# Kernel tuning notes

Hardware: AMD Instinct MI355X
Metric: run time of the kernel (lower is better)

Reference implementation:

```python
import jax, jax.numpy as jnp
import numpy as np

B, S, HID = 1, 4096, 2048
H, KVH, D = 8, 4, 256
QR, KR, VR = 6, 2, 2
WINDOW = 1024
SOFTCAP = 50.0
SCALING = 256.0 ** -0.5  # query_pre_attn_scalar ** -0.5
EPS = 1e-6
NEG = -2.3819763e38


def _rope(x, cos, sin):
    # x: [B,S,R,D]; cos/sin: [S,D//2] -> rotate interleaved complex pairs
    xr = x.reshape(*x.shape[:-1], D // 2, 2)
    x1, x2 = xr[..., 0], xr[..., 1]
    c = cos[None, :, None, :]
    s = sin[None, :, None, :]
    out = jnp.stack([x1 * c - x2 * s, x1 * s + x2 * c], axis=-1)
    return out.reshape(x.shape)


def _rmsnorm(x, w):
    var = jnp.mean(x * x, axis=-1, keepdims=True)
    return x * jax.lax.rsqrt(var + EPS) * (1.0 + w)


def setup_inputs() -> dict:
    key = jax.random.key(0)
    ks = jax.random.split(key, 12)
    sc = HID ** -0.5
    pos = np.arange(S, dtype=np.float32)
    inv = 1.0 / (10000.0 ** (np.arange(0, D, 2, dtype=np.float32) / D))
    fr = pos[:, None] * inv[None, :]
    return {
        'hidden_states': jax.random.normal(ks[0], (B, S, HID), jnp.float32),
        'freqs_cos': jnp.asarray(np.cos(fr), jnp.float32),
        'freqs_sin': jnp.asarray(np.sin(fr), jnp.float32),
        'W_A_q': jax.random.normal(ks[1], (H * QR, HID), jnp.float32) * sc,
        'W_A_k': jax.random.normal(ks[2], (KVH * KR, HID), jnp.float32) * sc,
        'W_A_v': jax.random.normal(ks[3], (KVH * VR, HID), jnp.float32) * sc,
        'W_B_q': jax.random.normal(ks[4], (QR * D, HID), jnp.float32) * sc,
        'W_B_k': jax.random.normal(ks[5], (KR * D, HID), jnp.float32) * sc,
        'W_B_v': jax.random.normal(ks[6], (VR * D, HID), jnp.float32) * sc,
        'W_o': jax.random.normal(ks[7], (HID, H * D), jnp.float32) * (H * D) ** -0.5,
        'q_norm_w': jnp.zeros((D,), jnp.float32),
        'k_norm_w': jnp.zeros((D,), jnp.float32),
        'k_cache_A': jnp.zeros((B, S, KVH, KR), jnp.float32),
        'k_cache_B': jnp.zeros((B, S, KR, D), jnp.float32),
        'v_cache_A': jnp.zeros((B, S, KVH, VR), jnp.float32),
        'v_cache_B': jnp.zeros((B, S, VR, D), jnp.float32),
        'kv_write_indices': jnp.arange(S, dtype=jnp.int32),
    }


def reference(hidden_states, freqs_cos, freqs_sin, W_A_q, W_A_k, W_A_v,
              W_B_q, W_B_k, W_B_v, W_o, q_norm_w, k_norm_w,
              k_cache_A, k_cache_B, v_cache_A, v_cache_B, kv_write_indices):
    x = hidden_states  # [B,S,HID]
    # factorized projections
    A_q = (x @ W_A_q.T).reshape(B, S, H, QR)
    A_k = (x @ W_A_k.T).reshape(B, S, KVH, KR)
    A_v = (x @ W_A_v.T).reshape(B, S, KVH, VR)
    B_q = (x @ W_B_q.T).reshape(B, S, QR, D)
    B_k = (x @ W_B_k.T).reshape(B, S, KR, D)
    B_v = (x @ W_B_v.T).reshape(B, S, VR, D)
    # RoPE on head-dim factors of Q and K
    B_q = _rope(B_q, freqs_cos, freqs_sin)
    B_k = _rope(B_k, freqs_cos, freqs_sin)
    # write factors into the TPA KV cache
    k_cache_A = k_cache_A.at[:, kv_write_indices].set(A_k)
    k_cache_B = k_cache_B.at[:, kv_write_indices].set(B_k)
    v_cache_A = v_cache_A.at[:, kv_write_indices].set(A_v)
    v_cache_B = v_cache_B.at[:, kv_write_indices].set(B_v)
    # reconstruct Q/K/V from rank-R tensor products (mean over rank)
    q = jnp.einsum('bshr,bsrd->bshd', A_q, B_q) / QR          # [B,S,H,D]
    k = jnp.einsum('btkr,btrd->btkd', k_cache_A, k_cache_B) / KR  # [B,T,KVH,D]
    v = jnp.einsum('btkr,btrd->btkd', v_cache_A, v_cache_B) / VR
    # QK RMSNorm
    q = _rmsnorm(q, q_norm_w)
    k = _rmsnorm(k, k_norm_w)
    # GQA: expand KV heads to query heads
    rep = H // KVH
    k = jnp.repeat(k, rep, axis=2)  # [B,T,H,D]
    v = jnp.repeat(v, rep, axis=2)
    # scores with softcapping + sliding-window causal mask
    scores = jnp.einsum('bshd,bthd->bhst', q * SCALING, k)
    scores = jnp.tanh(scores / SOFTCAP) * SOFTCAP
    q_pos = kv_write_indices[:, None]        # [S,1]
    k_pos = jnp.arange(S, dtype=jnp.int32)[None, :]  # [1,T]
    diff = q_pos - k_pos
    allowed = (diff >= 0) & (diff < WINDOW)
    scores = jnp.where(allowed[None, None], scores, NEG)
    probs = jax.nn.softmax(scores, axis=-1)
    out = jnp.einsum('bhst,bthd->bshd', probs, v).reshape(B, S, H * D)
    return out @ W_o.T
```

## Files before the change

kernel.cpp:

```cpp
#include <hip/hip_runtime.h>
#include <hip/hip_bf16.h>
#include <cstdint>
#include <cstddef>

constexpr int SEQ   = 4096;
constexpr int HIDN  = 2048;
constexpr int NHEAD = 8;
constexpr int NKVH  = 4;
constexpr int DH    = 256;
constexpr int NPROJ = 2624;
constexpr int NPROJP= 2816;
constexpr int WIN   = 1024;

typedef __attribute__((ext_vector_type(4))) float f32x4;
typedef __attribute__((ext_vector_type(8))) short bf16x8;
typedef unsigned short u16;

__device__ __forceinline__ u16 f2bf(float x) {
  union { float f; uint32_t u; } v; v.f = x;
  uint32_t r = v.u + 0x7fffu + ((v.u >> 16) & 1u);
  return (u16)(r >> 16);
}
__device__ __forceinline__ float bf2f(u16 v) {
  union { uint32_t u; float f; } w; w.u = (uint32_t)v << 16; return w.f;
}

__device__ __forceinline__ uint32_t cvtpk(float lo, float hi) {
  uint32_t r;
  asm("v_cvt_pk_bf16_f32 %0, %1, %2" : "=v"(r) : "v"(lo), "v"(hi));
  return r;
}

__device__ __forceinline__ void gl_lds16(const u16* g, u16* l) {
  __builtin_amdgcn_global_load_lds(
      (const __attribute__((address_space(1))) uint32_t*)g,
      (__attribute__((address_space(3))) uint32_t*)l, 16, 0, 0);
}

__device__ __forceinline__ void sync_vm() {
  asm volatile("s_waitcnt vmcnt(0)" ::: "memory");
  __builtin_amdgcn_s_barrier();
  __builtin_amdgcn_sched_barrier(0);
}

__device__ __forceinline__ void phase_barrier() {
  asm volatile("" ::: "memory");
  __builtin_amdgcn_s_barrier();
  __builtin_amdgcn_sched_barrier(0);
}

__device__ __forceinline__ int xcd_swz(int wg, int nwg) {
  const int q = nwg >> 3, r = nwg & 7;
  const int xcd = wg & 7, lo = wg >> 3;
  return (xcd < r ? xcd * (q + 1) : r * (q + 1) + (xcd - r) * q) + lo;
}

__global__ __launch_bounds__(256) void k_cvt(const float* __restrict__ src,
                                             u16* __restrict__ dst, int n4) {
  int i = blockIdx.x * 256 + threadIdx.x;
  if (i >= n4) return;
  float4 v = ((const float4*)src)[i];
  ushort4 o; o.x = f2bf(v.x); o.y = f2bf(v.y); o.z = f2bf(v.z); o.w = f2bf(v.w);
  ((ushort4*)dst)[i] = o;
}

__global__ __launch_bounds__(256) void k_wcat(
    const float* __restrict__ waq, const float* __restrict__ wak,
    const float* __restrict__ wav, const float* __restrict__ wbq,
    const float* __restrict__ wbk, const float* __restrict__ wbv,
    u16* __restrict__ wcat) {
  const int r = blockIdx.x;
  const int col0 = threadIdx.x * 8;
  u16* out = wcat + (size_t)r * HIDN + col0;
  const float* src = nullptr; int rr = 0;
  if      (r < 48)   { src = waq; rr = r; }
  else if (r < 56)   { src = wak; rr = r - 48; }
  else if (r < 64)   { src = wav; rr = r - 56; }
  else if (r < 1600) { src = wbq; rr = r - 64; }
  else if (r < 2112) { src = wbk; rr = r - 1600; }
  else if (r < 2624) { src = wbv; rr = r - 2112; }
  if (!src) {
    ushort4 z = {0,0,0,0}; ((ushort4*)out)[0] = z; ((ushort4*)out)[1] = z; return;
  }
  const float* s = src + (size_t)rr * HIDN + col0;
#pragma unroll
  for (int i = 0; i < 2; ++i) {
    float4 v = ((const float4*)s)[i];
    ushort4 o; o.x = f2bf(v.x); o.y = f2bf(v.y); o.z = f2bf(v.z); o.w = f2bf(v.w);
    ((ushort4*)out)[i] = o;
  }
}

template<int OBF16>
__global__ __launch_bounds__(512, 2)
void k_gemm256(const u16* __restrict__ A, const u16* __restrict__ Bm,
               void* __restrict__ Cv, int M, int N, int K) {
  __shared__ u16 lA[2][256 * 64];
  __shared__ u16 lB[2][256 * 64];
  const int tid = threadIdx.x;
  const int wid = tid >> 6, lane = tid & 63;
  const int l15 = lane & 15, g = lane >> 4;
  const int wr = wid >> 2, wc = wid & 3;
  const int nwg = gridDim.x * gridDim.y;
  int wg = xcd_swz(blockIdx.y * gridDim.x + blockIdx.x, nwg);
  const int m0 = (wg / gridDim.x) * 256, n0 = (wg % gridDim.x) * 256;

  f32x4 acc[8][4];
#pragma unroll
  for (int m = 0; m < 8; ++m)
#pragma unroll
    for (int n = 0; n < 4; ++n) acc[m][n] = (f32x4){0.f,0.f,0.f,0.f};
  const int NT = K >> 6;

  const int srow = tid >> 3;
  const int scc  = (tid & 7) ^ (srow & 7);
  const u16* ag = A  + (size_t)(m0 + srow) * K + scc * 8;
  const u16* bg = Bm + (size_t)(n0 + srow) * K + scc * 8;

  auto stB = [&](int buf, int kt) {
    const size_t ko = (size_t)kt << 6;
#pragma unroll
    for (int j = 0; j < 4; ++j)
      gl_lds16(bg + (size_t)(j*64) * K + ko, &lB[buf][j*4096 + wid*512]);
  };
  auto stA0 = [&](int buf, int kt) {
    const size_t ko = (size_t)kt << 6;
    gl_lds16(ag + ko,                   &lA[buf][wid*512]);
    gl_lds16(ag + (size_t)64 * K + ko,  &lA[buf][4096 + wid*512]);
  };
  auto stA1 = [&](int buf, int kt) {
    const size_t ko = (size_t)kt << 6;
    gl_lds16(ag + (size_t)128 * K + ko, &lA[buf][8192  + wid*512]);
    gl_lds16(ag + (size_t)192 * K + ko, &lA[buf][12288 + wid*512]);
  };

  const int sw8 = l15 & 7;
  int aoff[2], boff[2];
#pragma unroll
  for (int kk = 0; kk < 2; ++kk) {
    aoff[kk] = (wr*128 + l15)*64 + (((kk*4 + g) ^ sw8) << 3);
    boff[kk] = (wc*64  + l15)*64 + (((kk*4 + g) ^ sw8) << 3);
  }
  const u16* lAf = &lA[0][0];
  const u16* lBf = &lB[0][0];

  stB(0, 0); stA0(0, 0); stA1(0, 0);

  for (int t = 0; t < NT; ++t) {
    const int buf = t & 1, nb = buf ^ 1;
    const int ab = buf * 16384, bb = buf * 16384;
    const bool more = (t + 1 < NT);
    bf16x8 af[8], f0, f1;

    if (more) {
      stB(nb, t + 1);
      asm volatile("s_waitcnt vmcnt(4)" ::: "memory");
    } else {
      asm volatile("s_waitcnt vmcnt(0)" ::: "memory");
    }
    __builtin_amdgcn_s_barrier();
    __builtin_amdgcn_sched_barrier(0);
#pragma unroll
    for (int m = 0; m < 8; ++m) af[m] = *(const bf16x8*)&lAf[ab + aoff[0] + m*1024];
    f0 = *(const bf16x8*)&lBf[bb + boff[0]];
    f1 = *(const bf16x8*)&lBf[bb + boff[0] + 1024];
    __builtin_amdgcn_s_setprio(1);
#pragma unroll
    for (int m = 0; m < 8; ++m) {
      acc[m][0] = __builtin_amdgcn_mfma_f32_16x16x32_bf16(af[m], f0, acc[m][0], 0, 0, 0);
      acc[m][1] = __builtin_amdgcn_mfma_f32_16x16x32_bf16(af[m], f1, acc[m][1], 0, 0, 0);
    }
    __builtin_amdgcn_s_setprio(0);
    phase_barrier();

    f0 = *(const bf16x8*)&lBf[bb + boff[0] + 2048];
    f1 = *(const bf16x8*)&lBf[bb + boff[0] + 3072];
    if (more) stA0(nb, t + 1);
    phase_barrier();
    __builtin_amdgcn_s_setprio(1);
#pragma unroll
    for (int m = 0; m < 8; ++m) {
      acc[m][2] = __builtin_amdgcn_mfma_f32_16x16x32_bf16(af[m], f0, acc[m][2], 0, 0, 0);
      acc[m][3] = __builtin_amdgcn_mfma_f32_16x16x32_bf16(af[m], f1, acc[m][3], 0, 0, 0);
    }
    __builtin_amdgcn_s_setprio(0);
    phase_barrier();

#pragma unroll
    for (int m = 0; m < 8; ++m) af[m] = *(const bf16x8*)&lAf[ab + aoff[1] + m*1024];
    f0 = *(const bf16x8*)&lBf[bb + boff[1]];
    f1 = *(const bf16x8*)&lBf[bb + boff[1] + 1024];
    if (more) stA1(nb, t + 1);
    phase_barrier();
    __builtin_amdgcn_s_setprio(1);
#pragma unroll
    for (int m = 0; m < 8; ++m) {
      acc[m][0] = __builtin_amdgcn_mfma_f32_16x16x32_bf16(af[m], f0, acc[m][0], 0, 0, 0);
      acc[m][1] = __builtin_amdgcn_mfma_f32_16x16x32_bf16(af[m], f1, acc[m][1], 0, 0, 0);
    }
    __builtin_amdgcn_s_setprio(0);
    phase_barrier();

    f0 = *(const bf16x8*)&lBf[bb + boff[1] + 2048];
    f1 = *(const bf16x8*)&lBf[bb + boff[1] + 3072];
    phase_barrier();
    __builtin_amdgcn_s_setprio(1);
#pragma unroll
    for (int m = 0; m < 8; ++m) {
      acc[m][2] = __builtin_amdgcn_mfma_f32_16x16x32_bf16(af[m], f0, acc[m][2], 0, 0, 0);
      acc[m][3] = __builtin_amdgcn_mfma_f32_16x16x32_bf16(af[m], f1, acc[m][3], 0, 0, 0);
    }
    __builtin_amdgcn_s_setprio(0);
    phase_barrier();
  }

#pragma unroll
  for (int m = 0; m < 8; ++m)
#pragma unroll
    for (int n = 0; n < 4; ++n)
#pragma unroll
      for (int j = 0; j < 4; ++j) {
        const int row = m0 + wr*128 + m*16 + g*4 + j;
        const int col = n0 + wc*64 + n*16 + l15;
        if constexpr (OBF16) ((u16*)Cv)[(size_t)row * N + col] = f2bf(acc[m][n][j]);
        else                 ((float*)Cv)[(size_t)row * N + col] = acc[m][n][j];
      }
}

__global__ __launch_bounds__(256)
void k_qkv(const u16* __restrict__ Y, const float* __restrict__ cosT,
           const float* __restrict__ sinT, const float* __restrict__ qw,
           const float* __restrict__ kw, u16* __restrict__ q_s,
           u16* __restrict__ k_s, u16* __restrict__ v_s) {
  const int s = blockIdx.x;
  const int d = threadIdx.x;
  __shared__ float row[NPROJ];
  __shared__ float red[12][4];
  const u16* yr = Y + (size_t)s * NPROJP;
  for (int u4 = d; u4 < NPROJ/4; u4 += 256) {
    ushort4 v4 = ((const ushort4*)yr)[u4];
    row[u4*4+0] = bf2f(v4.x); row[u4*4+1] = bf2f(v4.y);
    row[u4*4+2] = bf2f(v4.z); row[u4*4+3] = bf2f(v4.w);
  }
  __syncthreads();
  const int i = d >> 1;
  const float cf = cosT[s * 128 + i];
  const float sf = sinT[s * 128 + i];
  const bool odd = d & 1;
  float bq[6], bk[2], bv[2];
#pragma unroll
  for (int r = 0; r < 6; ++r) {
    float x1 = row[64 + r*256 + 2*i], x2 = row[64 + r*256 + 2*i + 1];
    bq[r] = odd ? (x1*sf + x2*cf) : (x1*cf - x2*sf);
  }
#pragma unroll
  for (int r = 0; r < 2; ++r) {
    float x1 = row[1600 + r*256 + 2*i], x2 = row[1600 + r*256 + 2*i + 1];
    bk[r] = odd ? (x1*sf + x2*cf) : (x1*cf - x2*sf);
    bv[r] = row[2112 + r*256 + d];
  }
  float qv[8], kv[4], vv[4];
#pragma unroll
  for (int h = 0; h < 8; ++h) {
    float a = 0.f;
#pragma unroll
    for (int r = 0; r < 6; ++r) a += row[h*6 + r] * bq[r];
    qv[h] = a * (1.0f / 6.0f);
  }
#pragma unroll
  for (int c = 0; c < 4; ++c) {
    kv[c] = (row[48 + c*2]*bk[0] + row[48 + c*2 + 1]*bk[1]) * 0.5f;
    vv[c] = (row[56 + c*2]*bv[0] + row[56 + c*2 + 1]*bv[1]) * 0.5f;
  }
  const int lane = d & 63, wv = d >> 6;
#pragma unroll
  for (int t = 0; t < 12; ++t) {
    float x = (t < 8) ? qv[t] : kv[t - 8];
    float ss = x * x;
#pragma unroll
    for (int off = 32; off > 0; off >>= 1) ss += __shfl_xor(ss, off);
    if (lane == 0) red[t][wv] = ss;
  }
  __syncthreads();
  const float qwf = 1.0f + qw[d], kwf = 1.0f + kw[d];
#pragma unroll
  for (int h = 0; h < 8; ++h) {
    float v = red[h][0] + red[h][1] + red[h][2] + red[h][3];
    float r = rsqrtf(v * (1.0f/256.0f) + 1e-6f);
    q_s[((size_t)s*8 + h)*256 + d] = f2bf(qv[h] * r * qwf * 0.0625f);
  }
#pragma unroll
  for (int c = 0; c < 4; ++c) {
    float v = red[8+c][0] + red[8+c][1] + red[8+c][2] + red[8+c][3];
    float r = rsqrtf(v * (1.0f/256.0f) + 1e-6f);
    k_s[((size_t)s*4 + c)*256 + d] = f2bf(kv[c] * r * kwf);
    v_s[((size_t)s*4 + c)*256 + d] = f2bf(vv[c]);
  }
}

__global__ __launch_bounds__(256)
void k_vt(const u16* __restrict__ v_s, u16* __restrict__ vT) {
  __shared__ u16 tile[64][72];
  const int s0 = blockIdx.x * 64, d0 = blockIdx.y * 64, c = blockIdx.z;
  const int tid = threadIdx.x;
#pragma unroll
  for (int it = 0; it < 2; ++it) {
    const int u = it * 256 + tid;
    const int r = u >> 3, cc = u & 7;
    const u16* s = &v_s[(((size_t)(s0 + r))*4 + c)*256 + d0 + cc*8];
    ushort4 a = *(const ushort4*)s, b = *(const ushort4*)(s + 4);
    tile[r][cc*8+0]=a.x; tile[r][cc*8+1]=a.y; tile[r][cc*8+2]=a.z; tile[r][cc*8+3]=a.w;
    tile[r][cc*8+4]=b.x; tile[r][cc*8+5]=b.y; tile[r][cc*8+6]=b.z; tile[r][cc*8+7]=b.w;
  }
  __syncthreads();
#pragma unroll
  for (int it = 0; it < 2; ++it) {
    const int u = it * 256 + tid;
    const int dr = u >> 3, sc = u & 7;
    ushort4 a, b;
    a.x = tile[sc*8+0][dr]; a.y = tile[sc*8+1][dr]; a.z = tile[sc*8+2][dr]; a.w = tile[sc*8+3][dr];
    b.x = tile[sc*8+4][dr]; b.y = tile[sc*8+5][dr]; b.z = tile[sc*8+6][dr]; b.w = tile[sc*8+7][dr];
    u16* o = vT + ((size_t)c*256 + d0 + dr)*SEQ + s0 + sc*8;
    *(ushort4*)o = a; *(ushort4*)(o + 4) = b;
  }
}

__global__ __launch_bounds__(512, 2)
void k_attn(const u16* __restrict__ q_s, const u16* __restrict__ k_s,
            const u16* __restrict__ vT, const int* __restrict__ idx,
            u16* __restrict__ ao) {
  __shared__ u16 Kt[2][64 * 256];
  __shared__ u16 Vt[2][256 * 64];
  __shared__ u16 Pb[8][16 * 68];
  const int b = blockIdx.x;
  const int c = b & 3, qt = b >> 2;
  const int q0 = qt * 64;
  const int tid = threadIdx.x;
  const int wid = tid >> 6, lane = tid & 63;
  const int l15 = lane & 15, g = lane >> 4;
  const int h = 2*c + (wid >> 2);
  const int qsub = wid & 3;
  const int qrow = q0 + qsub*16 + l15;
  const int qpos = idx[qrow];

  bf16x8 qf[8];
  const u16* qb = q_s + ((size_t)qrow * 8 + h) * 256;
#pragma unroll
  for (int kk = 0; kk < 8; ++kk) qf[kk] = *(const bf16x8*)(qb + kk*32 + g*8);

  const int sw = l15 & 7;
  int kbase[8];
#pragma unroll
  for (int kk = 0; kk < 8; ++kk)
    kbase[kk] = l15*256 + ((((kk<<2)+g) ^ sw) << 3);
  u16* KtF = &Kt[0][0];
  u16* VtF = &Vt[0][0];
  u16* Pw  = &Pb[wid][0];

  f32x4 accO[16];
#pragma unroll
  for (int n = 0; n < 16; ++n) accO[n] = (f32x4){0.f,0.f,0.f,0.f};
  float mrun = -50.0f, lrun = 0.0f;

  int t0 = q0 - (WIN - 1); if (t0 < 0) t0 = 0;
  const int kt_lo = t0 >> 6, kt_hi = qt;

  const u16* kgp = k_s + (size_t)(kt_lo*64 + (tid>>5)) * 1024 + c*256
                   + (((tid & 31) ^ ((tid >> 5) & 7)) << 3);
  const u16* vgp = vT + (size_t)c*1048576 + (size_t)(tid>>3)*4096 + kt_lo*64
                   + (((tid & 7) ^ ((tid >> 3) & 7)) << 3);

  auto stage = [&](int buf) {
#pragma unroll
    for (int i = 0; i < 4; ++i)
      gl_lds16(kgp + i*16384,  &Kt[buf][(i*512 + wid*64) * 8]);
#pragma unroll
    for (int i = 0; i < 4; ++i)
      gl_lds16(vgp + i*262144, &Vt[buf][(i*512 + wid*64) * 8]);
  };

  stage(0);
  int cur = 0;
  for (int kt = kt_lo; kt <= kt_hi; ++kt) {
    const int k0 = kt << 6;
    sync_vm();
    if (kt < kt_hi) { kgp += 65536; vgp += 64; stage(cur ^ 1); }

    const int kco = cur * 16384;
    f32x4 sc[4];
#pragma unroll
    for (int nk = 0; nk < 4; ++nk) sc[nk] = (f32x4){0.f,0.f,0.f,0.f};
    __builtin_amdgcn_s_setprio(1);
#pragma unroll
    for (int nk = 0; nk < 4; ++nk)
#pragma unroll
      for (int kk = 0; kk < 8; ++kk) {
        bf16x8 kf = *(const bf16x8*)&KtF[kco + nk*4096 + kbase[kk]];
        sc[nk] = __builtin_amdgcn_mfma_f32_16x16x32_bf16(kf, qf[kk], sc[nk], 0, 0, 0);
      }
    __builtin_amdgcn_s_setprio(0);

    float tv[16];
#pragma unroll
    for (int nk = 0; nk < 4; ++nk)
#pragma unroll
      for (int j = 0; j < 4; ++j) {
        float u = __builtin_amdgcn_exp2f(sc[nk][j] * 0.05770780163555854f);
        tv[nk*4+j] = fmaf(-100.0f, __builtin_amdgcn_rcpf(1.0f + u), 50.0f);
      }
    if (kt == kt_hi) {
#pragma unroll
      for (int nk = 0; nk < 4; ++nk)
#pragma unroll
        for (int j = 0; j < 4; ++j)
          if (k0 + nk*16 + g*4 + j > qpos) tv[nk*4+j] = -1e38f;
    } else if (kt == kt_lo) {
#pragma unroll
      for (int nk = 0; nk < 4; ++nk)
#pragma unroll
        for (int j = 0; j < 4; ++j)
          if (qpos - (k0 + nk*16 + g*4 + j) > 1023) tv[nk*4+j] = -1e38f;
    }

    float tmax = tv[0];
#pragma unroll
    for (int t = 1; t < 16; ++t) tmax = fmaxf(tmax, tv[t]);
    if (__any(tmax > mrun + 8.0f)) {
      float tq = fmaxf(tmax, __shfl_xor(tmax, 16));
      tq = fmaxf(tq, __shfl_xor(tq, 32));
      const float mnew = fmaxf(mrun, tq);
      const float scale = __builtin_amdgcn_exp2f((mrun - mnew) * 1.442695041f);
      float scj[4];
#pragma unroll
      for (int j = 0; j < 4; ++j) scj[j] = __shfl(scale, g*4 + j);
#pragma unroll
      for (int n = 0; n < 16; ++n) {
        accO[n][0] *= scj[0]; accO[n][1] *= scj[1];
        accO[n][2] *= scj[2]; accO[n][3] *= scj[3];
      }
      lrun *= scale;
      mrun = mnew;
    }
    const float mr2 = mrun * 1.442695041f;
    float p[16];
#pragma unroll
    for (int t = 0; t < 16; ++t) {
      p[t] = __builtin_amdgcn_exp2f(fmaf(tv[t], 1.442695041f, -mr2));
      lrun += p[t];
    }

#pragma unroll
    for (int nk = 0; nk < 4; ++nk) {
      uint2 w = { cvtpk(p[nk*4+0], p[nk*4+1]), cvtpk(p[nk*4+2], p[nk*4+3]) };
      *(uint2*)&Pw[l15*68 + nk*16 + g*4] = w;
    }
    const int vco = cur * 16384;
    __builtin_amdgcn_s_setprio(1);
#pragma unroll
    for (int half = 0; half < 2; ++half) {
      bf16x8 pa = *(const bf16x8*)&Pw[l15*68 + half*32 + g*8];
#pragma unroll
      for (int n = 0; n < 16; ++n) {
        bf16x8 vf = *(const bf16x8*)&VtF[vco + (n*16 + l15)*64
                                         + ((((half<<2)+g) ^ sw) << 3)];
        accO[n] = __builtin_amdgcn_mfma_f32_16x16x32_bf16(pa, vf, accO[n], 0, 0, 0);
      }
    }
    __builtin_amdgcn_s_setprio(0);
    cur ^= 1;
  }

  lrun += __shfl_xor(lrun, 16);
  lrun += __shfl_xor(lrun, 32);
  const float linv = __builtin_amdgcn_rcpf(lrun);
  float lj[4];
#pragma unroll
  for (int j = 0; j < 4; ++j) lj[j] = __shfl(linv, g*4 + j);
#pragma unroll
  for (int n = 0; n < 16; ++n)
#pragma unroll
    for (int j = 0; j < 4; ++j) {
      const int r = q0 + qsub*16 + g*4 + j;
      ao[(size_t)r * HIDN + h*256 + n*16 + l15] = f2bf(accO[n][j] * lj[j]);
    }
}

extern "C" void kernel_launch(void* const* d_in, const int* in_sizes, int n_in,
                              void* d_out, int out_size, void* d_ws, size_t ws_size,
                              hipStream_t stream) {
  const float* x    = (const float*)d_in[0];
  const float* fcos = (const float*)d_in[1];
  const float* fsin = (const float*)d_in[2];
  const float* waq  = (const float*)d_in[3];
  const float* wak  = (const float*)d_in[4];
  const float* wav  = (const float*)d_in[5];
  const float* wbq  = (const float*)d_in[6];
  const float* wbk  = (const float*)d_in[7];
  const float* wbv  = (const float*)d_in[8];
  const float* wo   = (const float*)d_in[9];
  const float* qnw  = (const float*)d_in[10];
  const float* knw  = (const float*)d_in[11];
  const int*   idx  = (const int*)d_in[16];
  float* out = (float*)d_out;

  char* p = (char*)d_ws;
  u16*  xb   = (u16*)p;                 p += (size_t)SEQ*HIDN*2;
  u16*  wcat = (u16*)p;                 p += (size_t)NPROJP*HIDN*2;
  u16*  wob  = (u16*)p;                 p += (size_t)HIDN*HIDN*2;
  u16*  ypr  = (u16*)p;                 p += (size_t)SEQ*NPROJP*2;
  u16*  q_s  = (u16*)p;                 p += (size_t)SEQ*NHEAD*DH*2;
  u16*  k_s  = (u16*)p;                 p += (size_t)SEQ*NKVH*DH*2;
  u16*  v_s  = (u16*)p;                 p += (size_t)SEQ*NKVH*DH*2;
  u16*  vT   = (u16*)p;                 p += (size_t)SEQ*NKVH*DH*2;
  u16*  ao   = (u16*)p;                 p += (size_t)SEQ*HIDN*2;

  k_cvt <<<(SEQ*HIDN/4 + 255)/256, 256, 0, stream>>>(x, xb, SEQ*HIDN/4);
  k_cvt <<<(HIDN*HIDN/4 + 255)/256, 256, 0, stream>>>(wo, wob, HIDN*HIDN/4);
  k_wcat<<<NPROJP, 256, 0, stream>>>(waq, wak, wav, wbq, wbk, wbv, wcat);
  k_gemm256<1><<<dim3(NPROJP/256, SEQ/256), 512, 0, stream>>>(xb, wcat, ypr, SEQ, NPROJP, HIDN);
  k_qkv <<<SEQ, 256, 0, stream>>>(ypr, fcos, fsin, qnw, knw, q_s, k_s, v_s);
  k_vt  <<<dim3(SEQ/64, DH/64, NKVH), 256, 0, stream>>>(v_s, vT);
  k_attn<<<dim3(SEQ/64 * NKVH), 512, 0, stream>>>(q_s, k_s, vT, idx, ao);
  k_gemm256<0><<<dim3(HIDN/256, SEQ/256), 512, 0, stream>>>(ao, wob, out, SEQ, HIDN, HIDN);
}
```

Measured before the change: 253.6 us.

## Templatize GEMM tile shape and use 256x128 tiles for output projection

Generalizes the 256x256 GEMM kernel into a template over tile N width and warp layout. The output projection now uses 256x128 tiles with a 4x2 warp grid, doubling its block count from 128 to 256 so more CUs are filled. The inner loop is also restructured to load all four B fragments at once per k-half, dropping two phase barriers. The cost is less data reuse per tile and higher register use for the preloaded B fragments.

```diff
diff --git a/kernel.cpp b/kernel.cpp
--- a/kernel.cpp
+++ b/kernel.cpp
@@ -91,23 +91,25 @@
   }
 }
 
-template<int OBF16>
+template<int OBF16, int BN, int WM, int WN>
 __global__ __launch_bounds__(512, 2)
-void k_gemm256(const u16* __restrict__ A, const u16* __restrict__ Bm,
-               void* __restrict__ Cv, int M, int N, int K) {
+void k_gemm2(const u16* __restrict__ A, const u16* __restrict__ Bm,
+             void* __restrict__ Cv, int M, int N, int K) {
+  constexpr int MREP = 256 / WM / 16;
+  constexpr int BISS = BN / 64;
   __shared__ u16 lA[2][256 * 64];
-  __shared__ u16 lB[2][256 * 64];
+  __shared__ u16 lB[2][BN * 64];
   const int tid = threadIdx.x;
   const int wid = tid >> 6, lane = tid & 63;
   const int l15 = lane & 15, g = lane >> 4;
-  const int wr = wid >> 2, wc = wid & 3;
+  const int wr = wid / WN, wc = wid % WN;
   const int nwg = gridDim.x * gridDim.y;
   int wg = xcd_swz(blockIdx.y * gridDim.x + blockIdx.x, nwg);
-  const int m0 = (wg / gridDim.x) * 256, n0 = (wg % gridDim.x) * 256;
-
-  f32x4 acc[8][4];
-#pragma unroll
-  for (int m = 0; m < 8; ++m)
+  const int m0 = (wg / gridDim.x) * 256, n0 = (wg % gridDim.x) * BN;
+
+  f32x4 acc[MREP][4];
+#pragma unroll
+  for (int m = 0; m < MREP; ++m)
 #pragma unroll
     for (int n = 0; n < 4; ++n) acc[m][n] = (f32x4){0.f,0.f,0.f,0.f};
   const int NT = K >> 6;
@@ -120,7 +122,7 @@
   auto stB = [&](int buf, int kt) {
     const size_t ko = (size_t)kt << 6;
 #pragma unroll
-    for (int j = 0; j < 4; ++j)
+    for (int j = 0; j < BISS; ++j)
       gl_lds16(bg + (size_t)(j*64) * K + ko, &lB[buf][j*4096 + wid*512]);
   };
   auto stA0 = [&](int buf, int kt) {
@@ -135,11 +137,13 @@
   };
 
   const int sw8 = l15 & 7;
+  const int arow = wr * (256 / WM) + l15;
+  const int brow = wc * 64 + l15;
   int aoff[2], boff[2];
 #pragma unroll
   for (int kk = 0; kk < 2; ++kk) {
-    aoff[kk] = (wr*128 + l15)*64 + (((kk*4 + g) ^ sw8) << 3);
-    boff[kk] = (wc*64  + l15)*64 + (((kk*4 + g) ^ sw8) << 3);
+    aoff[kk] = arow*64 + (((kk*4 + g) ^ sw8) << 3);
+    boff[kk] = brow*64 + (((kk*4 + g) ^ sw8) << 3);
   }
   const u16* lAf = &lA[0][0];
   const u16* lBf = &lB[0][0];
@@ -148,79 +152,73 @@
 
   for (int t = 0; t < NT; ++t) {
     const int buf = t & 1, nb = buf ^ 1;
-    const int ab = buf * 16384, bb = buf * 16384;
+    const int ab = buf * 16384, bbo = buf * (BN * 64);
     const bool more = (t + 1 < NT);
-    bf16x8 af[8], f0, f1;
+    bf16x8 af[MREP], bf0[4], bf1[4];
 
     if (more) {
       stB(nb, t + 1);
-      asm volatile("s_waitcnt vmcnt(4)" ::: "memory");
+      if constexpr (BISS == 4) asm volatile("s_waitcnt vmcnt(4)" ::: "memory");
+      else                     asm volatile("s_waitcnt vmcnt(2)" ::: "memory");
     } else {
       asm volatile("s_waitcnt vmcnt(0)" ::: "memory");
     }
     __builtin_amdgcn_s_barrier();
     __builtin_amdgcn_sched_barrier(0);
 #pragma unroll
-    for (int m = 0; m < 8; ++m) af[m] = *(const bf16x8*)&lAf[ab + aoff[0] + m*1024];
-    f0 = *(const bf16x8*)&lBf[bb + boff[0]];
-    f1 = *(const bf16x8*)&lBf[bb + boff[0] + 1024];
+    for (int m = 0; m < MREP; ++m) af[m] = *(const bf16x8*)&lAf[ab + aoff[0] + m*1024];
+#pragma unroll
+    for (int n = 0; n < 4; ++n) bf0[n] = *(const bf16x8*)&lBf[bbo + boff[0] + n*1024];
     __builtin_amdgcn_s_setprio(1);
 #pragma unroll
-    for (int m = 0; m < 8; ++m) {
-      acc[m][0] = __builtin_amdgcn_mfma_f32_16x16x32_bf16(af[m], f0, acc[m][0], 0, 0, 0);
-      acc[m][1] = __builtin_amdgcn_mfma_f32_16x16x32_bf16(af[m], f1, acc[m][1], 0, 0, 0);
+    for (int m = 0; m < MREP; ++m) {
+      acc[m][0] = __builtin_amdgcn_mfma_f32_16x16x32_bf16(af[m], bf0[0], acc[m][0], 0, 0, 0);
+      acc[m][1] = __builtin_amdgcn_mfma_f32_16x16x32_bf16(af[m], bf0[1], acc[m][1], 0, 0, 0);
     }
     __builtin_amdgcn_s_setprio(0);
     phase_barrier();
 
-    f0 = *(const bf16x8*)&lBf[bb + boff[0] + 2048];
-    f1 = *(const bf16x8*)&lBf[bb + boff[0] + 3072];
     if (more) stA0(nb, t + 1);
-    phase_barrier();
     __builtin_amdgcn_s_setprio(1);
 #pragma unroll
-    for (int m = 0; m < 8; ++m) {
-      acc[m][2] = __builtin_amdgcn_mfma_f32_16x16x32_bf16(af[m], f0, acc[m][2], 0, 0, 0);
-      acc[m][3] = __builtin_amdgcn_mfma_f32_16x16x32_bf16(af[m], f1, acc[m][3], 0, 0, 0);
+    for (int m = 0; m < MREP; ++m) {
+      acc[m][2] = __builtin_amdgcn_mfma_f32_16x16x32_bf16(af[m], bf0[2], acc[m][2], 0, 0, 0);
+      acc[m][3] = __builtin_amdgcn_mfma_f32_16x16x32_bf16(af[m], bf0[3], acc[m][3], 0, 0, 0);
     }
     __builtin_amdgcn_s_setprio(0);
     phase_barrier();
 
-#pragma unroll
-    for (int m = 0; m < 8; ++m) af[m] = *(const bf16x8*)&lAf[ab + aoff[1] + m*1024];
-    f0 = *(const bf16x8*)&lBf[bb + boff[1]];
-    f1 = *(const bf16x8*)&lBf[bb + boff[1] + 1024];
     if (more) stA1(nb, t + 1);
-    phase_barrier();
+#pragma unroll
+    for (int m = 0; m < MREP; ++m) af[m] = *(const bf16x8*)&lAf[ab + aoff[1] + m*1024];
+#pragma unroll
+    for (int n = 0; n < 4; ++n) bf1[n] = *(const bf16x8*)&lBf[bbo + boff[1] + n*1024];
     __builtin_amdgcn_s_setprio(1);
 #pragma unroll
-    for (int m = 0; m < 8; ++m) {
-      acc[m][0] = __builtin_amdgcn_mfma_f32_16x16x32_bf16(af[m], f0, acc[m][0], 0, 0, 0);
-      acc[m][1] = __builtin_amdgcn_mfma_f32_16x16x32_bf16(af[m], f1, acc[m][1], 0, 0, 0);
+    for (int m = 0; m < MREP; ++m) {
+      acc[m][0] = __builtin_amdgcn_mfma_f32_16x16x32_bf16(af[m], bf1[0], acc[m][0], 0, 0, 0);
+      acc[m][1] = __builtin_amdgcn_mfma_f32_16x16x32_bf16(af[m], bf1[1], acc[m][1], 0, 0, 0);
     }
     __builtin_amdgcn_s_setprio(0);
     phase_barrier();
 
-    f0 = *(const bf16x8*)&lBf[bb + boff[1] + 2048];
-    f1 = *(const bf16x8*)&lBf[bb + boff[1] + 3072];
-    phase_barrier();
     __builtin_amdgcn_s_setprio(1);
 #pragma unroll
-    for (int m = 0; m < 8; ++m) {
-      acc[m][2] = __builtin_amdgcn_mfma_f32_16x16x32_bf16(af[m], f0, acc[m][2], 0, 0, 0);
-      acc[m][3] = __builtin_amdgcn_mfma_f32_16x16x32_bf16(af[m], f1, acc[m][3], 0, 0, 0);
+    for (int m = 0; m < MREP; ++m) {
+      acc[m][2] = __builtin_amdgcn_mfma_f32_16x16x32_bf16(af[m], bf1[2], acc[m][2], 0, 0, 0);
+      acc[m][3] = __builtin_amdgcn_mfma_f32_16x16x32_bf16(af[m], bf1[3], acc[m][3], 0, 0, 0);
     }
     __builtin_amdgcn_s_setprio(0);
     phase_barrier();
   }
 
 #pragma unroll
-  for (int m = 0; m < 8; ++m)
+  for (int m = 0; m < MREP; ++m)
 #pragma unroll
     for (int n = 0; n < 4; ++n)
 #pragma unroll
       for (int j = 0; j < 4; ++j) {
-        const int row = m0 + wr*128 + m*16 + g*4 + j;
+        const int row = m0 + wr*(256/WM) + m*16 + g*4 + j;
         const int col = n0 + wc*64 + n*16 + l15;
         if constexpr (OBF16) ((u16*)Cv)[(size_t)row * N + col] = f2bf(acc[m][n][j]);
         else                 ((float*)Cv)[(size_t)row * N + col] = acc[m][n][j];
@@ -517,9 +515,9 @@
   k_cvt <<<(SEQ*HIDN/4 + 255)/256, 256, 0, stream>>>(x, xb, SEQ*HIDN/4);
   k_cvt <<<(HIDN*HIDN/4 + 255)/256, 256, 0, stream>>>(wo, wob, HIDN*HIDN/4);
   k_wcat<<<NPROJP, 256, 0, stream>>>(waq, wak, wav, wbq, wbk, wbv, wcat);
-  k_gemm256<1><<<dim3(NPROJP/256, SEQ/256), 512, 0, stream>>>(xb, wcat, ypr, SEQ, NPROJP, HIDN);
+  k_gemm2<1, 256, 2, 4><<<dim3(NPROJP/256, SEQ/256), 512, 0, stream>>>(xb, wcat, ypr, SEQ, NPROJP, HIDN);
   k_qkv <<<SEQ, 256, 0, stream>>>(ypr, fcos, fsin, qnw, knw, q_s, k_s, v_s);
   k_vt  <<<dim3(SEQ/64, DH/64, NKVH), 256, 0, stream>>>(v_s, vT);
   k_attn<<<dim3(SEQ/64 * NKVH), 512, 0, stream>>>(q_s, k_s, vT, idx, ao);
-  k_gemm256<0><<<dim3(HIDN/256, SEQ/256), 512, 0, stream>>>(ao, wob, out, SEQ, HIDN, HIDN);
-}
+  k_gemm2<0, 128, 4, 2><<<dim3(HIDN/128, SEQ/256), 512, 0, stream>>>(ao, wob, out, SEQ, HIDN, HIDN);
+}
```

New measurement: 245.5 us. 1.03x faster.
